# Kernel tuning notes

Hardware: AMD Instinct MI355X
Metric: run time of the kernel (lower is better)

## Reference

```python
import math
import jax, jax.numpy as jnp
import numpy as np

WIDTH = 24
LAYERS = 4
MODES = (12, 12, 12)
FOURIER_K = 8
EPS = 1e-5  # torch GroupNorm default


def _posenc(B, Z, Y, X, dtype):
    z = jnp.linspace(-1.0, 1.0, Z, dtype=dtype)
    y = jnp.linspace(-1.0, 1.0, Y, dtype=dtype)
    x = jnp.linspace(-1.0, 1.0, X, dtype=dtype)
    zz, yy, xx = jnp.meshgrid(z, y, x, indexing='ij')
    feats = [zz, yy, xx]
    for k in range(1, FOURIER_K + 1):
        w = k * math.pi
        feats += [jnp.sin(w * zz), jnp.cos(w * zz),
                  jnp.sin(w * yy), jnp.cos(w * yy),
                  jnp.sin(w * xx), jnp.cos(w * xx)]
    pe = jnp.stack(feats, axis=0)  # [3 + 6K, Z, Y, X]
    return jnp.broadcast_to(pe[None], (B,) + pe.shape)


def _conv1x1(h, w, b):
    # h: [B,C,Z,Y,X], w: [O,C], b: [O]
    return jnp.einsum('bczyx,oc->bozyx', h, w) + b[None, :, None, None, None]


def _spectral(h, w_ri):
    # h: [B,C,Z,Y,X], w_ri: [C,O,mz,my,mx,2]
    B, C, Z, Y, X = h.shape
    mz, my, mx = MODES
    hf = jnp.fft.rfftn(h, axes=(-3, -2, -1))  # [B,C,Z,Y,X//2+1] complex
    wc = w_ri[..., 0] + 1j * w_ri[..., 1]
    out = jnp.einsum('bczyx,cozyx->bozyx', hf[:, :, :mz, :my, :mx], wc)
    full = jnp.zeros((B, wc.shape[1], Z, Y, X // 2 + 1), dtype=out.dtype)
    full = full.at[:, :, :mz, :my, :mx].set(out)
    return jnp.fft.irfftn(full, s=(Z, Y, X), axes=(-3, -2, -1)).astype(h.dtype)


def _depthwise3(h, w, b):
    # depthwise 3x3x3 conv, padding 1; w: [C,1,3,3,3]
    out = jax.lax.conv_general_dilated(
        h, w, window_strides=(1, 1, 1), padding='SAME',
        dimension_numbers=('NCDHW', 'OIDHW', 'NCDHW'),
        feature_group_count=WIDTH)
    return out + b[None, :, None, None, None]


def _groupnorm1(h, g, b):
    # GroupNorm with num_groups=1: normalize over (C,Z,Y,X) per sample
    m = jnp.mean(h, axis=(1, 2, 3, 4), keepdims=True)
    v = jnp.var(h, axis=(1, 2, 3, 4), keepdims=True)
    hn = (h - m) * jax.lax.rsqrt(v + EPS)
    return hn * g[None, :, None, None, None] + b[None, :, None, None, None]


def setup_inputs() -> dict:
    key = jax.random.key(0)
    ks = jax.random.split(key, 16)
    B, C_IN, Z, Y, X = 4, 3, 64, 64, 64
    mz, my, mx = MODES
    extra_c = 3 + 6 * FOURIER_K
    scale = 1.0 / (WIDTH * WIDTH)
    inp = {
        'x': jax.random.normal(ks[0], (B, C_IN, Z, Y, X), jnp.float32),
        'lift_w': jax.random.normal(ks[1], (WIDTH, C_IN + extra_c), jnp.float32) * 0.1,
        'lift_b': jax.random.normal(ks[2], (WIDTH,), jnp.float32) * 0.01,
        'spec_w': jax.random.normal(ks[3], (LAYERS, WIDTH, WIDTH, mz, my, mx, 2), jnp.float32) * scale,
        'ws_w': jax.random.normal(ks[4], (LAYERS, WIDTH, WIDTH), jnp.float32) * 0.1,
        'ws_b': jax.random.normal(ks[5], (LAYERS, WIDTH), jnp.float32) * 0.01,
        'loc_w': jax.random.normal(ks[6], (LAYERS, WIDTH, 1, 3, 3, 3), jnp.float32) * 0.1,
        'loc_b': jax.random.normal(ks[7], (LAYERS, WIDTH), jnp.float32) * 0.01,
        'gn_w': jnp.ones((LAYERS, WIDTH), jnp.float32),
        'gn_b': jnp.zeros((LAYERS, WIDTH), jnp.float32),
        'gammas': jnp.full((LAYERS,), 0.5, jnp.float32),
        'proj1_w': jax.random.normal(ks[8], (WIDTH, WIDTH), jnp.float32) * 0.1,
        'proj1_b': jax.random.normal(ks[9], (WIDTH,), jnp.float32) * 0.01,
        'proj2_w': jax.random.normal(ks[10], (1, WIDTH), jnp.float32) * 0.1,
        'proj2_b': jnp.zeros((1,), jnp.float32),
    }
    return inp


def reference(x, lift_w, lift_b, spec_w, ws_w, ws_b, loc_w, loc_b,
              gn_w, gn_b, gammas, proj1_w, proj1_b, proj2_w, proj2_b):
    B, _, Z, Y, X = x.shape
    pe = _posenc(B, Z, Y, X, x.dtype)
    xin = jnp.concatenate([x, pe], axis=1)
    h = _conv1x1(xin, lift_w, lift_b)
    for i in range(LAYERS):
        y = _spectral(h, spec_w[i]) + _conv1x1(h, ws_w[i], ws_b[i]) + _depthwise3(h, loc_w[i], loc_b[i])
        y = jax.nn.gelu(y, approximate=False)
        h = h + gammas[i] * y
        h = _groupnorm1(h, gn_w[i], gn_b[i])
    p = jax.nn.gelu(_conv1x1(h, proj1_w, proj1_b), approximate=False)
    return _conv1x1(p, proj2_w, proj2_b)  # [B,1,Z,Y,X]
```

## Files before the change

### kernel.cpp

```cpp
#include <hip/hip_runtime.h>
#include <hip/hip_bf16.h>
#include <math.h>


static constexpr int BN = 4;
static constexpr int CW = 24;
static constexpr int ZD = 64;
static constexpr size_t NPTS = 64ull * 64 * 64;
static constexpr int KM = 12;
static constexpr int KK2 = 144;
static constexpr int M3 = 1728;
static constexpr int NLAYERS = 4;

static constexpr size_t OFF_H     = 0;
static constexpr size_t OFF_PRE   = OFF_H   + (size_t)BN * CW * NPTS;
static constexpr size_t OFF_A1    = OFF_PRE + (size_t)BN * CW * NPTS;
static constexpr size_t OFF_A2    = OFF_A1  + (size_t)BN * CW * ZD * KM * ZD * 2;
static constexpr size_t OFF_HF    = OFF_A2  + (size_t)BN * CW * KK2 * ZD * 2;
static constexpr size_t OFF_OUT   = OFF_HF  + (size_t)BN * CW * M3 * 2;
static constexpr size_t OFF_AX    = OFF_OUT + (size_t)BN * CW * M3 * 2;
static constexpr size_t OFF_STATS = OFF_AX  + 3 * CW * 64;
static constexpr size_t OFF_GWGB  = OFF_STATS + NLAYERS * BN * 2;

__device__ __forceinline__ float gelu_exact(float y) {
  return 0.5f * y * (1.f + erff(y * 0.70710678118654752f));
}

__global__ void k_axis(const float* __restrict__ lw, float* __restrict__ ws) {
  int t = blockIdx.x * blockDim.x + threadIdx.x;
  if (blockIdx.x == 0 && threadIdx.x < BN * CW) {
    ws[OFF_GWGB + threadIdx.x * 2]     = 1.f;
    ws[OFF_GWGB + threadIdx.x * 2 + 1] = 0.f;
  }
  if (t >= 3 * CW * 64) return;
  int v = t & 63;
  int o = (t >> 6) % CW;
  int axis = t / (64 * CW);
  float val = -1.f + 2.f * (float)v / 63.f;
  float acc = lw[o * 54 + 3 + axis] * val;
  for (int k = 1; k <= 8; k++) {
    float s, c;
    sincosf((float)k * 3.14159265358979323846f * val, &s, &c);
    int base = 6 + 6 * (k - 1) + 2 * axis;
    acc += lw[o * 54 + base] * s + lw[o * 54 + base + 1] * c;
  }
  ws[OFF_AX + (size_t)axis * CW * 64 + o * 64 + v] = acc;
}

__global__ __launch_bounds__(64) void k_lift(const float* __restrict__ xin,
                                             const float* __restrict__ lw,
                                             const float* __restrict__ lb,
                                             float* __restrict__ ws) {
  int bid = blockIdx.x;
  int b = bid >> 12, z = (bid >> 6) & 63, y = bid & 63;
  int tx = threadIdx.x;
  size_t zyx = (size_t)z * 4096 + y * 64 + tx;
  float x0 = xin[(size_t)(b * 3 + 0) * NPTS + zyx];
  float x1 = xin[(size_t)(b * 3 + 1) * NPTS + zyx];
  float x2 = xin[(size_t)(b * 3 + 2) * NPTS + zyx];
  const float* az = ws + OFF_AX;
  const float* ay = az + CW * 64;
  const float* axt = ay + CW * 64;
  float* h = ws + OFF_H;
  for (int o = 0; o < CW; o++) {
    float acc = lb[o] + lw[o * 54 + 0] * x0 + lw[o * 54 + 1] * x1 +
                lw[o * 54 + 2] * x2 + az[o * 64 + z] + ay[o * 64 + y] + axt[o * 64 + tx];
    h[(size_t)(b * CW + o) * NPTS + zyx] = acc;
  }
}

__global__ void k_dftx(const float* __restrict__ hsrc, float* __restrict__ A1,
                       const float* __restrict__ gwgb) {
  __shared__ float pl[64][65];
  int bid = blockIdx.x;
  int bc = bid >> 6;
  float gw = gwgb[bc * 2], gb = gwgb[bc * 2 + 1];
  const float* src = hsrc + (size_t)bid * 4096;
  int t = threadIdx.x;
  for (int i = t; i < 4096; i += 256) pl[i >> 6][i & 63] = fmaf(src[i], gw, gb);
  __syncthreads();
  int q = t >> 6, y = t & 63;
  float C0, S0, C1, S1, C2, S2;
  sincosf(-6.283185307179586f * (float)q / 64.f, &S0, &C0);
  sincosf(-6.283185307179586f * (float)(q + 4) / 64.f, &S1, &C1);
  sincosf(-6.283185307179586f * (float)(q + 8) / 64.f, &S2, &C2);
  float r0 = 1.f, i0 = 0.f, r1 = 1.f, i1 = 0.f, r2 = 1.f, i2 = 0.f;
  float ar0 = 0.f, ai0 = 0.f, ar1 = 0.f, ai1 = 0.f, ar2 = 0.f, ai2 = 0.f;
  const float* row = pl[y];
  for (int xx = 0; xx < 64; xx++) {
    float v = row[xx];
    ar0 = fmaf(v, r0, ar0); ai0 = fmaf(v, i0, ai0);
    ar1 = fmaf(v, r1, ar1); ai1 = fmaf(v, i1, ai1);
    ar2 = fmaf(v, r2, ar2); ai2 = fmaf(v, i2, ai2);
    float nr;
    nr = r0 * C0 - i0 * S0; i0 = fmaf(r0, S0, i0 * C0); r0 = nr;
    nr = r1 * C1 - i1 * S1; i1 = fmaf(r1, S1, i1 * C1); r1 = nr;
    nr = r2 * C2 - i2 * S2; i2 = fmaf(r2, S2, i2 * C2); r2 = nr;
  }
  float2* dst = (float2*)A1 + (size_t)bid * KM * 64;
  dst[t]       = make_float2(ar0, ai0);
  dst[t + 256] = make_float2(ar1, ai1);
  dst[t + 512] = make_float2(ar2, ai2);
}

__global__ void k_dfty(const float* __restrict__ A1, float* __restrict__ A2) {
  __shared__ float lre[12][65], lim[12][65];
  int bid = blockIdx.x;
  int z = bid & 63, bc = bid >> 6;
  const float2* src = (const float2*)A1 + (size_t)bid * KM * 64;
  int t = threadIdx.x;
  for (int i = t; i < 768; i += 256) { float2 v = src[i]; lre[i >> 6][i & 63] = v.x; lim[i >> 6][i & 63] = v.y; }
  __syncthreads();
  if (t < KK2) {
    int ky = t / 12, kx = t % 12;
    float C, S;
    sincosf(-6.283185307179586f * (float)ky / 64.f, &S, &C);
    float r = 1.f, ir = 0.f;
    float re = 0.f, im = 0.f;
    for (int y = 0; y < 64; y++) {
      float ar = lre[kx][y], ai = lim[kx][y];
      re += ar * r - ai * ir;
      im += ai * r + ar * ir;
      float nr = r * C - ir * S; ir = fmaf(r, S, ir * C); r = nr;
    }
    ((float2*)A2)[((size_t)bc * KK2 + t) * 64 + z] = make_float2(re, im);
  }
}

__global__ void k_dftz(const float* __restrict__ A2, float* __restrict__ Hf) {
  __shared__ float lre[12][65], lim[12][65];
  int bid = blockIdx.x;
  int ky = bid % 12, bc = bid / 12;
  const float2* src = (const float2*)A2 + ((size_t)bc * KK2 + ky * 12) * 64;
  int t = threadIdx.x;
  for (int i = t; i < 768; i += 256) { float2 v = src[i]; lre[i >> 6][i & 63] = v.x; lim[i >> 6][i & 63] = v.y; }
  __syncthreads();
  if (t < KK2) {
    int kz = t / 12, kx = t % 12;
    float C, S;
    sincosf(-6.283185307179586f * (float)kz / 64.f, &S, &C);
    float r = 1.f, ir = 0.f;
    float re = 0.f, im = 0.f;
    for (int zz = 0; zz < 64; zz++) {
      float ar = lre[kx][zz], ai = lim[kx][zz];
      re += ar * r - ai * ir;
      im += ai * r + ar * ir;
      float nr = r * C - ir * S; ir = fmaf(r, S, ir * C); r = nr;
    }
    ((float2*)Hf)[(size_t)bc * M3 + kz * KK2 + ky * 12 + kx] = make_float2(re, im);
  }
}

__global__ void k_mix(const float* __restrict__ Hf, const float* __restrict__ specw,
                      float* __restrict__ Outb, int layer) {
  __shared__ float hre[24][64], him[24][64];
  int bid = blockIdx.x;
  int b = bid / 54, rem = bid % 54;
  int chunk = rem >> 1, og = rem & 1;
  int m0 = chunk * 64;
  int t = threadIdx.x;
  const float2* hf = (const float2*)Hf + (size_t)b * CW * M3;
  for (int i = t; i < 24 * 64; i += 256) {
    int c = i >> 6, m = i & 63;
    float2 v = hf[(size_t)c * M3 + m0 + m];
    hre[c][m] = v.x; him[c][m] = v.y;
  }
  __syncthreads();
  const float2* W2 = (const float2*)specw + (size_t)layer * 576 * M3;
  float2* outp = (float2*)Outb + (size_t)b * CW * M3;
  for (int p = t; p < 12 * 64; p += 256) {
    int o = og * 12 + (p >> 6), m = p & 63;
    int mg = m0 + m;
    float re = 0.f, im = 0.f;
    for (int c = 0; c < 24; c++) {
      float2 w = W2[(size_t)(c * 24 + o) * M3 + mg];
      float wr = w.x, wi = w.y;
      float ar = hre[c][m], ai = him[c][m];
      re += ar * wr - ai * wi;
      im += ar * wi + ai * wr;
    }
    int kx = mg % 12;
    float sc = (kx == 0 ? 1.f : 2.f) * (1.f / 262144.f);
    outp[(size_t)o * M3 + mg] = make_float2(re * sc, im * sc);
  }
}

__global__ void k_invz(const float* __restrict__ Outb, float* __restrict__ B1) {
  __shared__ float lre[1728], lim[1728];
  int bid = blockIdx.x;
  int bo = bid >> 2, zc = bid & 3;
  const float2* src = (const float2*)Outb + (size_t)bo * M3;
  int t = threadIdx.x;
  for (int i = t; i < 1728; i += 256) { float2 v = src[i]; lre[i] = v.x; lim[i] = v.y; }
  __syncthreads();
  float2* dst = (float2*)B1 + (size_t)bo * 64 * KK2 + (size_t)zc * 16 * KK2;
  for (int p = t; p < 16 * KK2; p += 256) {
    int z = zc * 16 + p / KK2, kk = p % KK2;
    float C, S;
    sincosf(6.283185307179586f * (float)z / 64.f, &S, &C);
    float r = 1.f, ir = 0.f;
    float re = 0.f, im = 0.f;
    for (int kz = 0; kz < 12; kz++) {
      float ar = lre[kz * KK2 + kk], ai = lim[kz * KK2 + kk];
      re += ar * r - ai * ir;
      im += ar * ir + ai * r;
      float nr = r * C - ir * S; ir = fmaf(r, S, ir * C); r = nr;
    }
    dst[p] = make_float2(re, im);
  }
}

__global__ void k_invy(const float* __restrict__ B1, float* __restrict__ B2) {
  __shared__ float lre[144], lim[144];
  int bid = blockIdx.x;
  const float2* src = (const float2*)B1 + (size_t)bid * KK2;
  int t = threadIdx.x;
  if (t < 144) { float2 v = src[t]; lre[t] = v.x; lim[t] = v.y; }
  __syncthreads();
  float2* dst = (float2*)B2 + (size_t)bid * 64 * KM;
  for (int p = t; p < 64 * KM; p += 256) {
    int y = p / KM, kx = p % KM;
    float C, S;
    sincosf(6.283185307179586f * (float)y / 64.f, &S, &C);
    float r = 1.f, ir = 0.f;
    float re = 0.f, im = 0.f;
    for (int ky = 0; ky < 12; ky++) {
      float ar = lre[ky * 12 + kx], ai = lim[ky * 12 + kx];
      re += ar * r - ai * ir;
      im += ar * ir + ai * r;
      float nr = r * C - ir * S; ir = fmaf(r, S, ir * C); r = nr;
    }
    dst[p] = make_float2(re, im);
  }
}

__global__ __launch_bounds__(256) void k_layer(const float* __restrict__ hsrc,
                                               const float* __restrict__ B2f,
                                               const float* __restrict__ wsw,
                                               const float* __restrict__ wsb,
                                               const float* __restrict__ locw,
                                               const float* __restrict__ locb,
                                               const float* __restrict__ gammas,
                                               const float* __restrict__ gwgb,
                                               float* __restrict__ pre,
                                               float* __restrict__ stats, int layer) {
  __shared__ __align__(16) float s_ws[576];
  __shared__ float s_loc[648];
  __shared__ __align__(16) float s_sp[2304];
  __shared__ float s_wsb[24], s_locb[24];
  __shared__ float s_gw[24], s_gb[24];
  __shared__ float s_ch[2][18][66];
  __shared__ float s_red[8];

  int bid = blockIdx.x;
  int b = bid >> 10, z = (bid >> 4) & 63, yt = bid & 15;
  int y0 = yt * 4;
  int tid = threadIdx.x;
  int tx = tid & 63, ty = tid >> 6;
  int y = y0 + ty;

  for (int i = tid; i < 576; i += 256) s_ws[i] = wsw[layer * 576 + i];
  for (int i = tid; i < 648; i += 256) s_loc[i] = locw[layer * 648 + i];
  const float2* b2 = (const float2*)B2f;
  for (int i = tid; i < 1152; i += 256) {
    int o = i / 48, rem = i % 48;
    int tyy = rem / 12, kxx = rem % 12;
    float2 v = b2[(((size_t)(b * CW + o) * 64 + z) * 64 + (y0 + tyy)) * KM + kxx];
    s_sp[((o * 4 + tyy) * 12 + kxx) * 2]     = v.x;
    s_sp[((o * 4 + tyy) * 12 + kxx) * 2 + 1] = v.y;
  }
  if (tid < 24) {
    s_wsb[tid] = wsb[layer * 24 + tid]; s_locb[tid] = locb[layer * 24 + tid];
    s_gw[tid] = gwgb[(b * CW + tid) * 2]; s_gb[tid] = gwgb[(b * CW + tid) * 2 + 1];
  }
  if (tid < 72) {
    int bf = tid / 36, rem = tid % 36;
    s_ch[bf][rem >> 1][(rem & 1) * 65] = 0.f;
  }
  __syncthreads();

  float cs[12], sn[12];
#pragma unroll
  for (int k = 0; k < 12; k++) {
    sincosf(6.283185307179586f * (float)((k * tx) & 63) / 64.f, &sn[k], &cs[k]);
  }

  float gamma = gammas[layer];
  size_t base_b = (size_t)b * CW * NPTS;
  size_t zyx = (size_t)z * 4096 + (size_t)y * 64 + tx;

  float hreg[24];
#pragma unroll
  for (int c = 0; c < 24; c++) hreg[c] = fmaf(hsrc[base_b + (size_t)c * NPTS + zyx], s_gw[c], s_gb[c]);

  int si[5]; size_t sgo[5]; bool svalid[5];
#pragma unroll
  for (int j = 0; j < 5; j++) {
    int i = tid + j * 256;
    si[j] = i;
    int rr = i >> 6, xx = i & 63;
    int z2 = z + rr / 6 - 1, y2 = y0 + (rr % 6) - 1;
    svalid[j] = (i < 1152) && ((unsigned)z2 < 64u) && ((unsigned)y2 < 64u);
    sgo[j] = (size_t)((unsigned)z2 & 63u) * 4096 + (size_t)((unsigned)y2 & 63u) * 64 + xx;
  }

#pragma unroll
  for (int j = 0; j < 5; j++) {
    float v = svalid[j] ? fmaf(hsrc[base_b + sgo[j]], s_gw[0], s_gb[0]) : 0.f;
    if (si[j] < 1152) s_ch[0][si[j] >> 6][(si[j] & 63) + 1] = v;
  }
  __syncthreads();

  float lsum = 0.f, lsq = 0.f;
  int cur = 0;
  for (int o = 0; o < 24; o++) {
    float r0 = 0.f, r1 = 0.f, r2 = 0.f, r3 = 0.f, r4 = 0.f;
    if (o < 23) {
      size_t nb = base_b + (size_t)(o + 1) * NPTS;
      if (svalid[0]) r0 = hsrc[nb + sgo[0]];
      if (svalid[1]) r1 = hsrc[nb + sgo[1]];
      if (svalid[2]) r2 = hsrc[nb + sgo[2]];
      if (svalid[3]) r3 = hsrc[nb + sgo[3]];
      if (svalid[4]) r4 = hsrc[nb + sgo[4]];
    }

    float hc = s_ch[cur][7 + ty][1 + tx];
    float dv = 0.f;
#pragma unroll
    for (int zi = 0; zi < 3; zi++) {
#pragma unroll
      for (int yi = 0; yi < 3; yi++) {
        const float* row = &s_ch[cur][zi * 6 + ty + yi][1 + tx];
        int wb = (zi * 3 + yi) * 3;
        dv += row[-1] * s_loc[o * 27 + wb] + row[0] * s_loc[o * 27 + wb + 1] + row[1] * s_loc[o * 27 + wb + 2];
      }
    }
    const float4* wsv = (const float4*)&s_ws[o * 24];
    float4 wa0 = wsv[0], wa1 = wsv[1], wa2 = wsv[2], wa3 = wsv[3], wa4 = wsv[4], wa5 = wsv[5];
    float wv = wa0.x * hreg[0]  + wa0.y * hreg[1]  + wa0.z * hreg[2]  + wa0.w * hreg[3]
             + wa1.x * hreg[4]  + wa1.y * hreg[5]  + wa1.z * hreg[6]  + wa1.w * hreg[7]
             + wa2.x * hreg[8]  + wa2.y * hreg[9]  + wa2.z * hreg[10] + wa2.w * hreg[11]
             + wa3.x * hreg[12] + wa3.y * hreg[13] + wa3.z * hreg[14] + wa3.w * hreg[15]
             + wa4.x * hreg[16] + wa4.y * hreg[17] + wa4.z * hreg[18] + wa4.w * hreg[19]
             + wa5.x * hreg[20] + wa5.y * hreg[21] + wa5.z * hreg[22] + wa5.w * hreg[23];
    const float4* spv = (const float4*)&s_sp[(o * 4 + ty) * 24];
    float4 p0 = spv[0], p1 = spv[1], p2 = spv[2], p3 = spv[3], p4 = spv[4], p5 = spv[5];
    float sp = p0.x * cs[0]  - p0.y * sn[0]  + p0.z * cs[1]  - p0.w * sn[1]
             + p1.x * cs[2]  - p1.y * sn[2]  + p1.z * cs[3]  - p1.w * sn[3]
             + p2.x * cs[4]  - p2.y * sn[4]  + p2.z * cs[5]  - p2.w * sn[5]
             + p3.x * cs[6]  - p3.y * sn[6]  + p3.z * cs[7]  - p3.w * sn[7]
             + p4.x * cs[8]  - p4.y * sn[8]  + p4.z * cs[9]  - p4.w * sn[9]
             + p5.x * cs[10] - p5.y * sn[10] + p5.z * cs[11] - p5.w * sn[11];
    float yv = sp + wv + s_wsb[o] + dv + s_locb[o];
    float pv = hc + gamma * gelu_exact(yv);
    pre[base_b + (size_t)o * NPTS + zyx] = pv;
    lsum += pv; lsq += pv * pv;

    if (o < 23) {
      int nbuf = cur ^ 1;
      float gwn = s_gw[o + 1], gbn = s_gb[o + 1];
      float w0 = svalid[0] ? fmaf(r0, gwn, gbn) : 0.f;
      float w1 = svalid[1] ? fmaf(r1, gwn, gbn) : 0.f;
      float w2 = svalid[2] ? fmaf(r2, gwn, gbn) : 0.f;
      float w3 = svalid[3] ? fmaf(r3, gwn, gbn) : 0.f;
      float w4 = svalid[4] ? fmaf(r4, gwn, gbn) : 0.f;
      if (si[0] < 1152) s_ch[nbuf][si[0] >> 6][(si[0] & 63) + 1] = w0;
      if (si[1] < 1152) s_ch[nbuf][si[1] >> 6][(si[1] & 63) + 1] = w1;
      if (si[2] < 1152) s_ch[nbuf][si[2] >> 6][(si[2] & 63) + 1] = w2;
      if (si[3] < 1152) s_ch[nbuf][si[3] >> 6][(si[3] & 63) + 1] = w3;
      if (si[4] < 1152) s_ch[nbuf][si[4] >> 6][(si[4] & 63) + 1] = w4;
    }
    __syncthreads();
    cur ^= 1;
  }

  for (int off = 32; off; off >>= 1) { lsum += __shfl_down(lsum, off); lsq += __shfl_down(lsq, off); }
  if (tx == 0) { s_red[ty * 2] = lsum; s_red[ty * 2 + 1] = lsq; }
  __syncthreads();
  if (tid == 0) {
    float a = s_red[0] + s_red[2] + s_red[4] + s_red[6];
    float q = s_red[1] + s_red[3] + s_red[5] + s_red[7];
    atomicAdd(&stats[(layer * BN + b) * 2], a);
    atomicAdd(&stats[(layer * BN + b) * 2 + 1], q);
  }
}

__global__ void k_gnstat(const float* __restrict__ stats, float* __restrict__ gwgb,
                         const float* __restrict__ gnw, const float* __restrict__ gnb,
                         int layer) {
  __shared__ float s_m[BN], s_r[BN];
  int t = threadIdx.x;
  if (t < BN) {
    float s1 = stats[(layer * BN + t) * 2];
    float s2 = stats[(layer * BN + t) * 2 + 1];
    float n = (float)(CW * NPTS);
    float mean = s1 / n;
    float var = s2 / n - mean * mean;
    s_m[t] = mean; s_r[t] = rsqrtf(var + 1e-5f);
  }
  __syncthreads();
  if (t < BN * CW) {
    int b = t / CW, c = t % CW;
    float gw = gnw[layer * CW + c] * s_r[b];
    float gb = gnb[layer * CW + c] - s_m[b] * gw;
    gwgb[((size_t)(layer + 1) * BN * CW + t) * 2]     = gw;
    gwgb[((size_t)(layer + 1) * BN * CW + t) * 2 + 1] = gb;
  }
}

__global__ __launch_bounds__(64) void k_proj(const float* __restrict__ h,
                                             const float* __restrict__ p1w,
                                             const float* __restrict__ p1b,
                                             const float* __restrict__ p2w,
                                             const float* __restrict__ p2b,
                                             const float* __restrict__ gwgb,
                                             float* __restrict__ out) {
  __shared__ float s_w[576], s_b[24], s_w2[24], s_gw[24], s_gb[24];
  int bid = blockIdx.x;
  int b = bid >> 12, z = (bid >> 6) & 63, y = bid & 63;
  int tx = threadIdx.x;
  for (int i = tx; i < 576; i += 64) s_w[i] = p1w[i];
  if (tx < 24) {
    s_b[tx] = p1b[tx]; s_w2[tx] = p2w[tx];
    s_gw[tx] = gwgb[(b * CW + tx) * 2]; s_gb[tx] = gwgb[(b * CW + tx) * 2 + 1];
  }
  __syncthreads();
  size_t zyx = (size_t)z * 4096 + y * 64 + tx;
  size_t base_b = (size_t)b * CW * NPTS;
  float hreg[24];
  for (int c = 0; c < 24; c++) hreg[c] = fmaf(h[base_b + (size_t)c * NPTS + zyx], s_gw[c], s_gb[c]);
  float acc = p2b[0];
  for (int o = 0; o < 24; o++) {
    float t = s_b[o];
#pragma unroll
    for (int c = 0; c < 24; c++) t += s_w[o * 24 + c] * hreg[c];
    acc += s_w2[o] * gelu_exact(t);
  }
  out[(size_t)b * NPTS + zyx] = acc;
}

extern "C" void kernel_launch(void* const* d_in, const int* in_sizes, int n_in,
                              void* d_out, int out_size, void* d_ws, size_t ws_size,
                              hipStream_t stream) {
  const float* xin    = (const float*)d_in[0];
  const float* lift_w = (const float*)d_in[1];
  const float* lift_b = (const float*)d_in[2];
  const float* spec_w = (const float*)d_in[3];
  const float* ws_w   = (const float*)d_in[4];
  const float* ws_b   = (const float*)d_in[5];
  const float* loc_w  = (const float*)d_in[6];
  const float* loc_b  = (const float*)d_in[7];
  const float* gn_w   = (const float*)d_in[8];
  const float* gn_b   = (const float*)d_in[9];
  const float* gammas = (const float*)d_in[10];
  const float* p1w    = (const float*)d_in[11];
  const float* p1b    = (const float*)d_in[12];
  const float* p2w    = (const float*)d_in[13];
  const float* p2b    = (const float*)d_in[14];
  float* ws = (float*)d_ws;
  float* out = (float*)d_out;

  float* gwgb = ws + OFF_GWGB;
  float* state[2] = { ws + OFF_H, ws + OFF_PRE };

  hipMemsetAsync(ws + OFF_STATS, 0, (NLAYERS * BN * 2) * sizeof(float), stream);

  k_axis<<<18, 256, 0, stream>>>(lift_w, ws);
  k_lift<<<BN * 4096, 64, 0, stream>>>(xin, lift_w, lift_b, ws);

  for (int l = 0; l < NLAYERS; l++) {
    const float* src = state[l & 1];
    float* dst = state[(l & 1) ^ 1];
    const float* slot = gwgb + (size_t)l * BN * CW * 2;
    k_dftx<<<BN * CW * 64, 256, 0, stream>>>(src, ws + OFF_A1, slot);
    k_dfty<<<BN * CW * 64, 256, 0, stream>>>(ws + OFF_A1, ws + OFF_A2);
    k_dftz<<<BN * CW * 12, 256, 0, stream>>>(ws + OFF_A2, ws + OFF_HF);
    k_mix<<<BN * 54, 256, 0, stream>>>(ws + OFF_HF, spec_w, ws + OFF_OUT, l);
    k_invz<<<BN * CW * 4, 256, 0, stream>>>(ws + OFF_OUT, ws + OFF_A2);
    k_invy<<<BN * CW * 64, 256, 0, stream>>>(ws + OFF_A2, ws + OFF_A1);
    k_layer<<<BN * 1024, 256, 0, stream>>>(src, ws + OFF_A1, ws_w, ws_b, loc_w, loc_b,
                                           gammas, slot, dst, ws + OFF_STATS, l);
    k_gnstat<<<1, 128, 0, stream>>>(ws + OFF_STATS, gwgb, gn_w, gn_b, l);
  }
  k_proj<<<BN * 4096, 64, 0, stream>>>(state[0], p1w, p1b, p2w, p2b,
                                       gwgb + (size_t)NLAYERS * BN * CW * 2, out);
}
```

Baseline: 1.652 ms.

## Fuse y/z forward DFTs, inline GroupNorm affine, pair channels in layer kernel

Merges the separate y and z truncated-DFT kernels into one kernel that keeps the intermediate in shared memory, so the A2 global round trip and one launch go away. Drops the k_gnstat kernel and has each consumer compute the GroupNorm scale and shift directly from the accumulated stats. The layer kernel now handles two output channels per iteration with packed float2 weights and 4 staging buffers, which halves loop trips and barriers. The cost is more shared memory and registers per block in k_layer, plus redundant stat math in every block.

```diff
diff --git a/kernel.cpp b/kernel.cpp
--- a/kernel.cpp
+++ b/kernel.cpp
@@ -11,6 +11,10 @@
 static constexpr int KK2 = 144;
 static constexpr int M3 = 1728;
 static constexpr int NLAYERS = 4;
+static constexpr float GN_N = 6291456.0f;
+
+typedef float v2f __attribute__((ext_vector_type(2)));
+static __device__ __forceinline__ v2f mk2(float a, float b) { v2f r; r.x = a; r.y = b; return r; }
 
 static constexpr size_t OFF_H     = 0;
 static constexpr size_t OFF_PRE   = OFF_H   + (size_t)BN * CW * NPTS;
@@ -20,18 +24,28 @@
 static constexpr size_t OFF_OUT   = OFF_HF  + (size_t)BN * CW * M3 * 2;
 static constexpr size_t OFF_AX    = OFF_OUT + (size_t)BN * CW * M3 * 2;
 static constexpr size_t OFF_STATS = OFF_AX  + 3 * CW * 64;
-static constexpr size_t OFF_GWGB  = OFF_STATS + NLAYERS * BN * 2;
 
 __device__ __forceinline__ float gelu_exact(float y) {
   return 0.5f * y * (1.f + erff(y * 0.70710678118654752f));
 }
 
+__device__ __forceinline__ void gn_affine(const float* stats, const float* gnw,
+                                          const float* gnb, int lm1, int b, int c,
+                                          float& gw, float& gb) {
+  gw = 1.f; gb = 0.f;
+  if (lm1 >= 0) {
+    float s1 = stats[(lm1 * BN + b) * 2];
+    float s2 = stats[(lm1 * BN + b) * 2 + 1];
+    float mean = s1 / GN_N;
+    float var = s2 / GN_N - mean * mean;
+    float rstd = rsqrtf(var + 1e-5f);
+    gw = gnw[lm1 * CW + c] * rstd;
+    gb = gnb[lm1 * CW + c] - mean * gw;
+  }
+}
+
 __global__ void k_axis(const float* __restrict__ lw, float* __restrict__ ws) {
   int t = blockIdx.x * blockDim.x + threadIdx.x;
-  if (blockIdx.x == 0 && threadIdx.x < BN * CW) {
-    ws[OFF_GWGB + threadIdx.x * 2]     = 1.f;
-    ws[OFF_GWGB + threadIdx.x * 2 + 1] = 0.f;
-  }
   if (t >= 3 * CW * 64) return;
   int v = t & 63;
   int o = (t >> 6) % CW;
@@ -70,11 +84,13 @@
 }
 
 __global__ void k_dftx(const float* __restrict__ hsrc, float* __restrict__ A1,
-                       const float* __restrict__ gwgb) {
+                       const float* __restrict__ stats, const float* __restrict__ gnw,
+                       const float* __restrict__ gnb, int layer) {
   __shared__ float pl[64][65];
   int bid = blockIdx.x;
   int bc = bid >> 6;
-  float gw = gwgb[bc * 2], gb = gwgb[bc * 2 + 1];
+  float gw, gb;
+  gn_affine(stats, gnw, gnb, layer - 1, bc / CW, bc % CW, gw, gb);
   const float* src = hsrc + (size_t)bid * 4096;
   int t = threadIdx.x;
   for (int i = t; i < 4096; i += 256) pl[i >> 6][i & 63] = fmaf(src[i], gw, gb);
@@ -103,46 +119,42 @@
   dst[t + 512] = make_float2(ar2, ai2);
 }
 
-__global__ void k_dfty(const float* __restrict__ A1, float* __restrict__ A2) {
-  __shared__ float lre[12][65], lim[12][65];
-  int bid = blockIdx.x;
-  int z = bid & 63, bc = bid >> 6;
-  const float2* src = (const float2*)A1 + (size_t)bid * KM * 64;
+__global__ void k_dftyz(const float* __restrict__ A1, float* __restrict__ Hf) {
+  __shared__ float in_re[64][65], in_im[64][65];
+  __shared__ float o1_re[12][65], o1_im[12][65];
+  int bid = blockIdx.x;
+  int kx = bid % 12, bc = bid / 12;
   int t = threadIdx.x;
-  for (int i = t; i < 768; i += 256) { float2 v = src[i]; lre[i >> 6][i & 63] = v.x; lim[i >> 6][i & 63] = v.y; }
-  __syncthreads();
-  if (t < KK2) {
-    int ky = t / 12, kx = t % 12;
+  const float2* src = (const float2*)A1;
+  for (int i = t; i < 4096; i += 256) {
+    int z = i >> 6, y = i & 63;
+    float2 v = src[((size_t)(bc * 64 + z)) * 768 + kx * 64 + y];
+    in_re[z][y] = v.x; in_im[z][y] = v.y;
+  }
+  __syncthreads();
+  for (int i = t; i < 768; i += 256) {
+    int z = i / 12, ky = i % 12;
     float C, S;
     sincosf(-6.283185307179586f * (float)ky / 64.f, &S, &C);
     float r = 1.f, ir = 0.f;
     float re = 0.f, im = 0.f;
     for (int y = 0; y < 64; y++) {
-      float ar = lre[kx][y], ai = lim[kx][y];
+      float ar = in_re[z][y], ai = in_im[z][y];
       re += ar * r - ai * ir;
       im += ai * r + ar * ir;
       float nr = r * C - ir * S; ir = fmaf(r, S, ir * C); r = nr;
     }
-    ((float2*)A2)[((size_t)bc * KK2 + t) * 64 + z] = make_float2(re, im);
-  }
-}
-
-__global__ void k_dftz(const float* __restrict__ A2, float* __restrict__ Hf) {
-  __shared__ float lre[12][65], lim[12][65];
-  int bid = blockIdx.x;
-  int ky = bid % 12, bc = bid / 12;
-  const float2* src = (const float2*)A2 + ((size_t)bc * KK2 + ky * 12) * 64;
-  int t = threadIdx.x;
-  for (int i = t; i < 768; i += 256) { float2 v = src[i]; lre[i >> 6][i & 63] = v.x; lim[i >> 6][i & 63] = v.y; }
+    o1_re[ky][z] = re; o1_im[ky][z] = im;
+  }
   __syncthreads();
   if (t < KK2) {
-    int kz = t / 12, kx = t % 12;
+    int kz = t / 12, ky = t % 12;
     float C, S;
     sincosf(-6.283185307179586f * (float)kz / 64.f, &S, &C);
     float r = 1.f, ir = 0.f;
     float re = 0.f, im = 0.f;
     for (int zz = 0; zz < 64; zz++) {
-      float ar = lre[kx][zz], ai = lim[kx][zz];
+      float ar = o1_re[ky][zz], ai = o1_im[ky][zz];
       re += ar * r - ai * ir;
       im += ai * r + ar * ir;
       float nr = r * C - ir * S; ir = fmaf(r, S, ir * C); r = nr;
@@ -241,15 +253,15 @@
                                                const float* __restrict__ locw,
                                                const float* __restrict__ locb,
                                                const float* __restrict__ gammas,
-                                               const float* __restrict__ gwgb,
+                                               const float* __restrict__ gnw,
+                                               const float* __restrict__ gnb,
                                                float* __restrict__ pre,
                                                float* __restrict__ stats, int layer) {
-  __shared__ __align__(16) float s_ws[576];
-  __shared__ float s_loc[648];
-  __shared__ __align__(16) float s_sp[2304];
-  __shared__ float s_wsb[24], s_locb[24];
-  __shared__ float s_gw[24], s_gb[24];
-  __shared__ float s_ch[2][18][66];
+  __shared__ __align__(16) float s_ws2[576];
+  __shared__ __align__(8)  float s_loc2[1296];
+  __shared__ __align__(16) float s_sp2[2304];
+  __shared__ float s_wsb[24], s_locb[24], s_gw[24], s_gb[24];
+  __shared__ float s_ch[4][18][66];
   __shared__ float s_red[8];
 
   int bid = blockIdx.x;
@@ -259,21 +271,30 @@
   int tx = tid & 63, ty = tid >> 6;
   int y = y0 + ty;
 
-  for (int i = tid; i < 576; i += 256) s_ws[i] = wsw[layer * 576 + i];
-  for (int i = tid; i < 648; i += 256) s_loc[i] = locw[layer * 648 + i];
+  for (int i = tid; i < 576; i += 256) {
+    int o = i / 24, c = i % 24;
+    s_ws2[((o >> 1) * 24 + c) * 2 + (o & 1)] = wsw[layer * 576 + i];
+  }
+  for (int i = tid; i < 648; i += 256) {
+    int o = i / 27, tap = i % 27;
+    s_loc2[((o >> 1) * 27 + tap) * 2 + (o & 1)] = locw[layer * 648 + i];
+  }
   const float2* b2 = (const float2*)B2f;
   for (int i = tid; i < 1152; i += 256) {
     int o = i / 48, rem = i % 48;
     int tyy = rem / 12, kxx = rem % 12;
     float2 v = b2[(((size_t)(b * CW + o) * 64 + z) * 64 + (y0 + tyy)) * KM + kxx];
-    s_sp[((o * 4 + tyy) * 12 + kxx) * 2]     = v.x;
-    s_sp[((o * 4 + tyy) * 12 + kxx) * 2 + 1] = v.y;
+    int base = (((o >> 1) * 4 + tyy) * 12 + kxx) * 4;
+    s_sp2[base + (o & 1)]     = v.x;
+    s_sp2[base + 2 + (o & 1)] = v.y;
   }
   if (tid < 24) {
     s_wsb[tid] = wsb[layer * 24 + tid]; s_locb[tid] = locb[layer * 24 + tid];
-    s_gw[tid] = gwgb[(b * CW + tid) * 2]; s_gb[tid] = gwgb[(b * CW + tid) * 2 + 1];
-  }
-  if (tid < 72) {
+    float gw, gb;
+    gn_affine(stats, gnw, gnb, layer - 1, b, tid, gw, gb);
+    s_gw[tid] = gw; s_gb[tid] = gb;
+  }
+  if (tid < 144) {
     int bf = tid / 36, rem = tid % 36;
     s_ch[bf][rem >> 1][(rem & 1) * 65] = 0.f;
   }
@@ -306,72 +327,87 @@
 
 #pragma unroll
   for (int j = 0; j < 5; j++) {
-    float v = svalid[j] ? fmaf(hsrc[base_b + sgo[j]], s_gw[0], s_gb[0]) : 0.f;
-    if (si[j] < 1152) s_ch[0][si[j] >> 6][(si[j] & 63) + 1] = v;
+    float vA = svalid[j] ? fmaf(hsrc[base_b + sgo[j]], s_gw[0], s_gb[0]) : 0.f;
+    float vB = svalid[j] ? fmaf(hsrc[base_b + NPTS + sgo[j]], s_gw[1], s_gb[1]) : 0.f;
+    if (si[j] < 1152) {
+      s_ch[0][si[j] >> 6][(si[j] & 63) + 1] = vA;
+      s_ch[1][si[j] >> 6][(si[j] & 63) + 1] = vB;
+    }
   }
   __syncthreads();
 
   float lsum = 0.f, lsq = 0.f;
-  int cur = 0;
-  for (int o = 0; o < 24; o++) {
-    float r0 = 0.f, r1 = 0.f, r2 = 0.f, r3 = 0.f, r4 = 0.f;
-    if (o < 23) {
-      size_t nb = base_b + (size_t)(o + 1) * NPTS;
-      if (svalid[0]) r0 = hsrc[nb + sgo[0]];
-      if (svalid[1]) r1 = hsrc[nb + sgo[1]];
-      if (svalid[2]) r2 = hsrc[nb + sgo[2]];
-      if (svalid[3]) r3 = hsrc[nb + sgo[3]];
-      if (svalid[4]) r4 = hsrc[nb + sgo[4]];
-    }
-
-    float hc = s_ch[cur][7 + ty][1 + tx];
-    float dv = 0.f;
+#pragma unroll 1
+  for (int op = 0; op < 12; op++) {
+    int tb = (op & 1) * 2;
+    float r0=0.f,r1=0.f,r2=0.f,r3=0.f,r4=0.f,r5=0.f,r6=0.f,r7=0.f,r8=0.f,r9=0.f;
+    if (op < 11) {
+      size_t nbA = base_b + (size_t)(2 * op + 2) * NPTS;
+      size_t nbB = nbA + NPTS;
+      if (svalid[0]) { r0 = hsrc[nbA + sgo[0]]; r5 = hsrc[nbB + sgo[0]]; }
+      if (svalid[1]) { r1 = hsrc[nbA + sgo[1]]; r6 = hsrc[nbB + sgo[1]]; }
+      if (svalid[2]) { r2 = hsrc[nbA + sgo[2]]; r7 = hsrc[nbB + sgo[2]]; }
+      if (svalid[3]) { r3 = hsrc[nbA + sgo[3]]; r8 = hsrc[nbB + sgo[3]]; }
+      if (svalid[4]) { r4 = hsrc[nbA + sgo[4]]; r9 = hsrc[nbB + sgo[4]]; }
+    }
+
+    const float* t0 = &s_ch[tb][0][0];
+    const float* t1 = &s_ch[tb + 1][0][0];
+    v2f dv = mk2(0.f, 0.f), wv = mk2(0.f, 0.f), sp = mk2(0.f, 0.f);
 #pragma unroll
     for (int zi = 0; zi < 3; zi++) {
 #pragma unroll
       for (int yi = 0; yi < 3; yi++) {
-        const float* row = &s_ch[cur][zi * 6 + ty + yi][1 + tx];
-        int wb = (zi * 3 + yi) * 3;
-        dv += row[-1] * s_loc[o * 27 + wb] + row[0] * s_loc[o * 27 + wb + 1] + row[1] * s_loc[o * 27 + wb + 2];
+        int ro = (zi * 6 + ty + yi) * 66 + 1 + tx;
+        float a0m = t0[ro - 1], a00 = t0[ro], a0p = t0[ro + 1];
+        float a1m = t1[ro - 1], a10 = t1[ro], a1p = t1[ro + 1];
+        const v2f* lp = (const v2f*)&s_loc2[(op * 27 + (zi * 3 + yi) * 3) * 2];
+        dv += mk2(a0m, a1m) * lp[0];
+        dv += mk2(a00, a10) * lp[1];
+        dv += mk2(a0p, a1p) * lp[2];
       }
     }
-    const float4* wsv = (const float4*)&s_ws[o * 24];
-    float4 wa0 = wsv[0], wa1 = wsv[1], wa2 = wsv[2], wa3 = wsv[3], wa4 = wsv[4], wa5 = wsv[5];
-    float wv = wa0.x * hreg[0]  + wa0.y * hreg[1]  + wa0.z * hreg[2]  + wa0.w * hreg[3]
-             + wa1.x * hreg[4]  + wa1.y * hreg[5]  + wa1.z * hreg[6]  + wa1.w * hreg[7]
-             + wa2.x * hreg[8]  + wa2.y * hreg[9]  + wa2.z * hreg[10] + wa2.w * hreg[11]
-             + wa3.x * hreg[12] + wa3.y * hreg[13] + wa3.z * hreg[14] + wa3.w * hreg[15]
-             + wa4.x * hreg[16] + wa4.y * hreg[17] + wa4.z * hreg[18] + wa4.w * hreg[19]
-             + wa5.x * hreg[20] + wa5.y * hreg[21] + wa5.z * hreg[22] + wa5.w * hreg[23];
-    const float4* spv = (const float4*)&s_sp[(o * 4 + ty) * 24];
-    float4 p0 = spv[0], p1 = spv[1], p2 = spv[2], p3 = spv[3], p4 = spv[4], p5 = spv[5];
-    float sp = p0.x * cs[0]  - p0.y * sn[0]  + p0.z * cs[1]  - p0.w * sn[1]
-             + p1.x * cs[2]  - p1.y * sn[2]  + p1.z * cs[3]  - p1.w * sn[3]
-             + p2.x * cs[4]  - p2.y * sn[4]  + p2.z * cs[5]  - p2.w * sn[5]
-             + p3.x * cs[6]  - p3.y * sn[6]  + p3.z * cs[7]  - p3.w * sn[7]
-             + p4.x * cs[8]  - p4.y * sn[8]  + p4.z * cs[9]  - p4.w * sn[9]
-             + p5.x * cs[10] - p5.y * sn[10] + p5.z * cs[11] - p5.w * sn[11];
-    float yv = sp + wv + s_wsb[o] + dv + s_locb[o];
-    float pv = hc + gamma * gelu_exact(yv);
-    pre[base_b + (size_t)o * NPTS + zyx] = pv;
-    lsum += pv; lsq += pv * pv;
-
-    if (o < 23) {
-      int nbuf = cur ^ 1;
-      float gwn = s_gw[o + 1], gbn = s_gb[o + 1];
-      float w0 = svalid[0] ? fmaf(r0, gwn, gbn) : 0.f;
-      float w1 = svalid[1] ? fmaf(r1, gwn, gbn) : 0.f;
-      float w2 = svalid[2] ? fmaf(r2, gwn, gbn) : 0.f;
-      float w3 = svalid[3] ? fmaf(r3, gwn, gbn) : 0.f;
-      float w4 = svalid[4] ? fmaf(r4, gwn, gbn) : 0.f;
-      if (si[0] < 1152) s_ch[nbuf][si[0] >> 6][(si[0] & 63) + 1] = w0;
-      if (si[1] < 1152) s_ch[nbuf][si[1] >> 6][(si[1] & 63) + 1] = w1;
-      if (si[2] < 1152) s_ch[nbuf][si[2] >> 6][(si[2] & 63) + 1] = w2;
-      if (si[3] < 1152) s_ch[nbuf][si[3] >> 6][(si[3] & 63) + 1] = w3;
-      if (si[4] < 1152) s_ch[nbuf][si[4] >> 6][(si[4] & 63) + 1] = w4;
+    const v2f* wp = (const v2f*)&s_ws2[op * 48];
+#pragma unroll
+    for (int c = 0; c < 24; c++) wv += wp[c] * hreg[c];
+    const float4* spp = (const float4*)&s_sp2[(op * 4 + ty) * 48];
+#pragma unroll
+    for (int kx = 0; kx < 12; kx++) {
+      float4 q = spp[kx];
+      sp += mk2(q.x, q.y) * cs[kx];
+      sp -= mk2(q.z, q.w) * sn[kx];
+    }
+    int o0 = 2 * op, o1 = 2 * op + 1;
+    float hc0 = t0[(7 + ty) * 66 + 1 + tx];
+    float hc1 = t1[(7 + ty) * 66 + 1 + tx];
+    v2f yv = sp + wv + dv;
+    float pv0 = hc0 + gamma * gelu_exact(yv.x + s_wsb[o0] + s_locb[o0]);
+    float pv1 = hc1 + gamma * gelu_exact(yv.y + s_wsb[o1] + s_locb[o1]);
+    pre[base_b + (size_t)o0 * NPTS + zyx] = pv0;
+    pre[base_b + (size_t)o1 * NPTS + zyx] = pv1;
+    lsum += pv0 + pv1; lsq += pv0 * pv0 + pv1 * pv1;
+
+    if (op < 11) {
+      int nb = tb ^ 2;
+      float gwa = s_gw[o0 + 2], gba = s_gb[o0 + 2];
+      float gwb = s_gw[o1 + 2], gbb = s_gb[o1 + 2];
+      float wA0 = svalid[0] ? fmaf(r0, gwa, gba) : 0.f;
+      float wA1 = svalid[1] ? fmaf(r1, gwa, gba) : 0.f;
+      float wA2 = svalid[2] ? fmaf(r2, gwa, gba) : 0.f;
+      float wA3 = svalid[3] ? fmaf(r3, gwa, gba) : 0.f;
+      float wA4 = svalid[4] ? fmaf(r4, gwa, gba) : 0.f;
+      float wB0 = svalid[0] ? fmaf(r5, gwb, gbb) : 0.f;
+      float wB1 = svalid[1] ? fmaf(r6, gwb, gbb) : 0.f;
+      float wB2 = svalid[2] ? fmaf(r7, gwb, gbb) : 0.f;
+      float wB3 = svalid[3] ? fmaf(r8, gwb, gbb) : 0.f;
+      float wB4 = svalid[4] ? fmaf(r9, gwb, gbb) : 0.f;
+      if (si[0] < 1152) { s_ch[nb][si[0] >> 6][(si[0] & 63) + 1] = wA0; s_ch[nb + 1][si[0] >> 6][(si[0] & 63) + 1] = wB0; }
+      if (si[1] < 1152) { s_ch[nb][si[1] >> 6][(si[1] & 63) + 1] = wA1; s_ch[nb + 1][si[1] >> 6][(si[1] & 63) + 1] = wB1; }
+      if (si[2] < 1152) { s_ch[nb][si[2] >> 6][(si[2] & 63) + 1] = wA2; s_ch[nb + 1][si[2] >> 6][(si[2] & 63) + 1] = wB2; }
+      if (si[3] < 1152) { s_ch[nb][si[3] >> 6][(si[3] & 63) + 1] = wA3; s_ch[nb + 1][si[3] >> 6][(si[3] & 63) + 1] = wB3; }
+      if (si[4] < 1152) { s_ch[nb][si[4] >> 6][(si[4] & 63) + 1] = wA4; s_ch[nb + 1][si[4] >> 6][(si[4] & 63) + 1] = wB4; }
     }
     __syncthreads();
-    cur ^= 1;
   }
 
   for (int off = 32; off; off >>= 1) { lsum += __shfl_down(lsum, off); lsq += __shfl_down(lsq, off); }
@@ -385,35 +421,14 @@
   }
 }
 
-__global__ void k_gnstat(const float* __restrict__ stats, float* __restrict__ gwgb,
-                         const float* __restrict__ gnw, const float* __restrict__ gnb,
-                         int layer) {
-  __shared__ float s_m[BN], s_r[BN];
-  int t = threadIdx.x;
-  if (t < BN) {
-    float s1 = stats[(layer * BN + t) * 2];
-    float s2 = stats[(layer * BN + t) * 2 + 1];
-    float n = (float)(CW * NPTS);
-    float mean = s1 / n;
-    float var = s2 / n - mean * mean;
-    s_m[t] = mean; s_r[t] = rsqrtf(var + 1e-5f);
-  }
-  __syncthreads();
-  if (t < BN * CW) {
-    int b = t / CW, c = t % CW;
-    float gw = gnw[layer * CW + c] * s_r[b];
-    float gb = gnb[layer * CW + c] - s_m[b] * gw;
-    gwgb[((size_t)(layer + 1) * BN * CW + t) * 2]     = gw;
-    gwgb[((size_t)(layer + 1) * BN * CW + t) * 2 + 1] = gb;
-  }
-}
-
 __global__ __launch_bounds__(64) void k_proj(const float* __restrict__ h,
                                              const float* __restrict__ p1w,
                                              const float* __restrict__ p1b,
                                              const float* __restrict__ p2w,
                                              const float* __restrict__ p2b,
-                                             const float* __restrict__ gwgb,
+                                             const float* __restrict__ stats,
+                                             const float* __restrict__ gnw,
+                                             const float* __restrict__ gnb,
                                              float* __restrict__ out) {
   __shared__ float s_w[576], s_b[24], s_w2[24], s_gw[24], s_gb[24];
   int bid = blockIdx.x;
@@ -422,7 +437,9 @@
   for (int i = tx; i < 576; i += 64) s_w[i] = p1w[i];
   if (tx < 24) {
     s_b[tx] = p1b[tx]; s_w2[tx] = p2w[tx];
-    s_gw[tx] = gwgb[(b * CW + tx) * 2]; s_gb[tx] = gwgb[(b * CW + tx) * 2 + 1];
+    float gw, gb;
+    gn_affine(stats, gnw, gnb, NLAYERS - 1, b, tx, gw, gb);
+    s_gw[tx] = gw; s_gb[tx] = gb;
   }
   __syncthreads();
   size_t zyx = (size_t)z * 4096 + y * 64 + tx;
@@ -460,10 +477,10 @@
   float* ws = (float*)d_ws;
   float* out = (float*)d_out;
 
-  float* gwgb = ws + OFF_GWGB;
+  float* stats = ws + OFF_STATS;
   float* state[2] = { ws + OFF_H, ws + OFF_PRE };
 
-  hipMemsetAsync(ws + OFF_STATS, 0, (NLAYERS * BN * 2) * sizeof(float), stream);
+  hipMemsetAsync(stats, 0, (NLAYERS * BN * 2) * sizeof(float), stream);
 
   k_axis<<<18, 256, 0, stream>>>(lift_w, ws);
   k_lift<<<BN * 4096, 64, 0, stream>>>(xin, lift_w, lift_b, ws);
@@ -471,17 +488,14 @@
   for (int l = 0; l < NLAYERS; l++) {
     const float* src = state[l & 1];
     float* dst = state[(l & 1) ^ 1];
-    const float* slot = gwgb + (size_t)l * BN * CW * 2;
-    k_dftx<<<BN * CW * 64, 256, 0, stream>>>(src, ws + OFF_A1, slot);
-    k_dfty<<<BN * CW * 64, 256, 0, stream>>>(ws + OFF_A1, ws + OFF_A2);
-    k_dftz<<<BN * CW * 12, 256, 0, stream>>>(ws + OFF_A2, ws + OFF_HF);
+    k_dftx<<<BN * CW * 64, 256, 0, stream>>>(src, ws + OFF_A1, stats, gn_w, gn_b, l);
+    k_dftyz<<<BN * CW * 12, 256, 0, stream>>>(ws + OFF_A1, ws + OFF_HF);
     k_mix<<<BN * 54, 256, 0, stream>>>(ws + OFF_HF, spec_w, ws + OFF_OUT, l);
     k_invz<<<BN * CW * 4, 256, 0, stream>>>(ws + OFF_OUT, ws + OFF_A2);
     k_invy<<<BN * CW * 64, 256, 0, stream>>>(ws + OFF_A2, ws + OFF_A1);
     k_layer<<<BN * 1024, 256, 0, stream>>>(src, ws + OFF_A1, ws_w, ws_b, loc_w, loc_b,
-                                           gammas, slot, dst, ws + OFF_STATS, l);
-    k_gnstat<<<1, 128, 0, stream>>>(ws + OFF_STATS, gwgb, gn_w, gn_b, l);
+                                           gammas, gn_w, gn_b, dst, stats, l);
   }
   k_proj<<<BN * 4096, 64, 0, stream>>>(state[0], p1w, p1b, p2w, p2b,
-                                       gwgb + (size_t)NLAYERS * BN * CW * 2, out);
-}
+                                       stats, gn_w, gn_b, out);
+}
```

New measurement: 1.715 ms. 3.8% more time.

## Fuse y/z forward DFTs, inline GroupNorm affine, widen lift/proj blocks

Applied to the files above, without the earlier changes.

Merges the separate y- and z-direction truncated DFT kernels into one kernel that keeps the intermediate in shared memory, dropping the A2 round trip and one launch per layer. Removes the k_gnstat kernel by having each consumer compute the GroupNorm scale and shift directly from the accumulated stats. Widens the lift and projection kernels from 64-thread to 256-thread blocks. The fused DFT kernel launches only BN*CW*12 blocks that each hold a larger shared buffer, which may lower parallelism.

```diff
diff --git a/kernel.cpp b/kernel.cpp
--- a/kernel.cpp
+++ b/kernel.cpp
@@ -11,6 +11,7 @@
 static constexpr int KK2 = 144;
 static constexpr int M3 = 1728;
 static constexpr int NLAYERS = 4;
+static constexpr float GN_N = 6291456.0f;
 
 static constexpr size_t OFF_H     = 0;
 static constexpr size_t OFF_PRE   = OFF_H   + (size_t)BN * CW * NPTS;
@@ -20,18 +21,28 @@
 static constexpr size_t OFF_OUT   = OFF_HF  + (size_t)BN * CW * M3 * 2;
 static constexpr size_t OFF_AX    = OFF_OUT + (size_t)BN * CW * M3 * 2;
 static constexpr size_t OFF_STATS = OFF_AX  + 3 * CW * 64;
-static constexpr size_t OFF_GWGB  = OFF_STATS + NLAYERS * BN * 2;
 
 __device__ __forceinline__ float gelu_exact(float y) {
   return 0.5f * y * (1.f + erff(y * 0.70710678118654752f));
 }
 
+__device__ __forceinline__ void gn_affine(const float* stats, const float* gnw,
+                                          const float* gnb, int lm1, int b, int c,
+                                          float& gw, float& gb) {
+  gw = 1.f; gb = 0.f;
+  if (lm1 >= 0) {
+    float s1 = stats[(lm1 * BN + b) * 2];
+    float s2 = stats[(lm1 * BN + b) * 2 + 1];
+    float mean = s1 / GN_N;
+    float var = s2 / GN_N - mean * mean;
+    float rstd = rsqrtf(var + 1e-5f);
+    gw = gnw[lm1 * CW + c] * rstd;
+    gb = gnb[lm1 * CW + c] - mean * gw;
+  }
+}
+
 __global__ void k_axis(const float* __restrict__ lw, float* __restrict__ ws) {
   int t = blockIdx.x * blockDim.x + threadIdx.x;
-  if (blockIdx.x == 0 && threadIdx.x < BN * CW) {
-    ws[OFF_GWGB + threadIdx.x * 2]     = 1.f;
-    ws[OFF_GWGB + threadIdx.x * 2 + 1] = 0.f;
-  }
   if (t >= 3 * CW * 64) return;
   int v = t & 63;
   int o = (t >> 6) % CW;
@@ -47,13 +58,15 @@
   ws[OFF_AX + (size_t)axis * CW * 64 + o * 64 + v] = acc;
 }
 
-__global__ __launch_bounds__(64) void k_lift(const float* __restrict__ xin,
-                                             const float* __restrict__ lw,
-                                             const float* __restrict__ lb,
-                                             float* __restrict__ ws) {
-  int bid = blockIdx.x;
-  int b = bid >> 12, z = (bid >> 6) & 63, y = bid & 63;
-  int tx = threadIdx.x;
+__global__ __launch_bounds__(256) void k_lift(const float* __restrict__ xin,
+                                              const float* __restrict__ lw,
+                                              const float* __restrict__ lb,
+                                              float* __restrict__ ws) {
+  int bid = blockIdx.x;
+  int b = bid >> 10, z = (bid >> 4) & 63, yt = bid & 15;
+  int tid = threadIdx.x;
+  int tx = tid & 63, ty = tid >> 6;
+  int y = yt * 4 + ty;
   size_t zyx = (size_t)z * 4096 + y * 64 + tx;
   float x0 = xin[(size_t)(b * 3 + 0) * NPTS + zyx];
   float x1 = xin[(size_t)(b * 3 + 1) * NPTS + zyx];
@@ -70,11 +83,13 @@
 }
 
 __global__ void k_dftx(const float* __restrict__ hsrc, float* __restrict__ A1,
-                       const float* __restrict__ gwgb) {
+                       const float* __restrict__ stats, const float* __restrict__ gnw,
+                       const float* __restrict__ gnb, int layer) {
   __shared__ float pl[64][65];
   int bid = blockIdx.x;
   int bc = bid >> 6;
-  float gw = gwgb[bc * 2], gb = gwgb[bc * 2 + 1];
+  float gw, gb;
+  gn_affine(stats, gnw, gnb, layer - 1, bc / CW, bc % CW, gw, gb);
   const float* src = hsrc + (size_t)bid * 4096;
   int t = threadIdx.x;
   for (int i = t; i < 4096; i += 256) pl[i >> 6][i & 63] = fmaf(src[i], gw, gb);
@@ -103,46 +118,42 @@
   dst[t + 512] = make_float2(ar2, ai2);
 }
 
-__global__ void k_dfty(const float* __restrict__ A1, float* __restrict__ A2) {
-  __shared__ float lre[12][65], lim[12][65];
-  int bid = blockIdx.x;
-  int z = bid & 63, bc = bid >> 6;
-  const float2* src = (const float2*)A1 + (size_t)bid * KM * 64;
+__global__ void k_dftyz(const float* __restrict__ A1, float* __restrict__ Hf) {
+  __shared__ float in_re[64][65], in_im[64][65];
+  __shared__ float o1_re[12][65], o1_im[12][65];
+  int bid = blockIdx.x;
+  int kx = bid % 12, bc = bid / 12;
   int t = threadIdx.x;
-  for (int i = t; i < 768; i += 256) { float2 v = src[i]; lre[i >> 6][i & 63] = v.x; lim[i >> 6][i & 63] = v.y; }
-  __syncthreads();
-  if (t < KK2) {
-    int ky = t / 12, kx = t % 12;
+  const float2* src = (const float2*)A1;
+  for (int i = t; i < 4096; i += 256) {
+    int z = i >> 6, y = i & 63;
+    float2 v = src[((size_t)(bc * 64 + z)) * 768 + kx * 64 + y];
+    in_re[z][y] = v.x; in_im[z][y] = v.y;
+  }
+  __syncthreads();
+  for (int i = t; i < 768; i += 256) {
+    int z = i / 12, ky = i % 12;
     float C, S;
     sincosf(-6.283185307179586f * (float)ky / 64.f, &S, &C);
     float r = 1.f, ir = 0.f;
     float re = 0.f, im = 0.f;
     for (int y = 0; y < 64; y++) {
-      float ar = lre[kx][y], ai = lim[kx][y];
+      float ar = in_re[z][y], ai = in_im[z][y];
       re += ar * r - ai * ir;
       im += ai * r + ar * ir;
       float nr = r * C - ir * S; ir = fmaf(r, S, ir * C); r = nr;
     }
-    ((float2*)A2)[((size_t)bc * KK2 + t) * 64 + z] = make_float2(re, im);
-  }
-}
-
-__global__ void k_dftz(const float* __restrict__ A2, float* __restrict__ Hf) {
-  __shared__ float lre[12][65], lim[12][65];
-  int bid = blockIdx.x;
-  int ky = bid % 12, bc = bid / 12;
-  const float2* src = (const float2*)A2 + ((size_t)bc * KK2 + ky * 12) * 64;
-  int t = threadIdx.x;
-  for (int i = t; i < 768; i += 256) { float2 v = src[i]; lre[i >> 6][i & 63] = v.x; lim[i >> 6][i & 63] = v.y; }
+    o1_re[ky][z] = re; o1_im[ky][z] = im;
+  }
   __syncthreads();
   if (t < KK2) {
-    int kz = t / 12, kx = t % 12;
+    int kz = t / 12, ky = t % 12;
     float C, S;
     sincosf(-6.283185307179586f * (float)kz / 64.f, &S, &C);
     float r = 1.f, ir = 0.f;
     float re = 0.f, im = 0.f;
     for (int zz = 0; zz < 64; zz++) {
-      float ar = lre[kx][zz], ai = lim[kx][zz];
+      float ar = o1_re[ky][zz], ai = o1_im[ky][zz];
       re += ar * r - ai * ir;
       im += ai * r + ar * ir;
       float nr = r * C - ir * S; ir = fmaf(r, S, ir * C); r = nr;
@@ -241,7 +252,8 @@
                                                const float* __restrict__ locw,
                                                const float* __restrict__ locb,
                                                const float* __restrict__ gammas,
-                                               const float* __restrict__ gwgb,
+                                               const float* __restrict__ gnw,
+                                               const float* __restrict__ gnb,
                                                float* __restrict__ pre,
                                                float* __restrict__ stats, int layer) {
   __shared__ __align__(16) float s_ws[576];
@@ -271,7 +283,9 @@
   }
   if (tid < 24) {
     s_wsb[tid] = wsb[layer * 24 + tid]; s_locb[tid] = locb[layer * 24 + tid];
-    s_gw[tid] = gwgb[(b * CW + tid) * 2]; s_gb[tid] = gwgb[(b * CW + tid) * 2 + 1];
+    float gw, gb;
+    gn_affine(stats, gnw, gnb, layer - 1, b, tid, gw, gb);
+    s_gw[tid] = gw; s_gb[tid] = gb;
   }
   if (tid < 72) {
     int bf = tid / 36, rem = tid % 36;
@@ -385,49 +399,33 @@
   }
 }
 
-__global__ void k_gnstat(const float* __restrict__ stats, float* __restrict__ gwgb,
-                         const float* __restrict__ gnw, const float* __restrict__ gnb,
-                         int layer) {
-  __shared__ float s_m[BN], s_r[BN];
-  int t = threadIdx.x;
-  if (t < BN) {
-    float s1 = stats[(layer * BN + t) * 2];
-    float s2 = stats[(layer * BN + t) * 2 + 1];
-    float n = (float)(CW * NPTS);
-    float mean = s1 / n;
-    float var = s2 / n - mean * mean;
-    s_m[t] = mean; s_r[t] = rsqrtf(var + 1e-5f);
-  }
-  __syncthreads();
-  if (t < BN * CW) {
-    int b = t / CW, c = t % CW;
-    float gw = gnw[layer * CW + c] * s_r[b];
-    float gb = gnb[layer * CW + c] - s_m[b] * gw;
-    gwgb[((size_t)(layer + 1) * BN * CW + t) * 2]     = gw;
-    gwgb[((size_t)(layer + 1) * BN * CW + t) * 2 + 1] = gb;
-  }
-}
-
-__global__ __launch_bounds__(64) void k_proj(const float* __restrict__ h,
-                                             const float* __restrict__ p1w,
-                                             const float* __restrict__ p1b,
-                                             const float* __restrict__ p2w,
-                                             const float* __restrict__ p2b,
-                                             const float* __restrict__ gwgb,
-                                             float* __restrict__ out) {
+__global__ __launch_bounds__(256) void k_proj(const float* __restrict__ h,
+                                              const float* __restrict__ p1w,
+                                              const float* __restrict__ p1b,
+                                              const float* __restrict__ p2w,
+                                              const float* __restrict__ p2b,
+                                              const float* __restrict__ stats,
+                                              const float* __restrict__ gnw,
+                                              const float* __restrict__ gnb,
+                                              float* __restrict__ out) {
   __shared__ float s_w[576], s_b[24], s_w2[24], s_gw[24], s_gb[24];
   int bid = blockIdx.x;
-  int b = bid >> 12, z = (bid >> 6) & 63, y = bid & 63;
-  int tx = threadIdx.x;
-  for (int i = tx; i < 576; i += 64) s_w[i] = p1w[i];
-  if (tx < 24) {
-    s_b[tx] = p1b[tx]; s_w2[tx] = p2w[tx];
-    s_gw[tx] = gwgb[(b * CW + tx) * 2]; s_gb[tx] = gwgb[(b * CW + tx) * 2 + 1];
-  }
-  __syncthreads();
-  size_t zyx = (size_t)z * 4096 + y * 64 + tx;
+  int b = bid >> 10, z = (bid >> 4) & 63, yt = bid & 15;
+  int tid = threadIdx.x;
+  int tx = tid & 63, ty = tid >> 6;
+  int y = yt * 4 + ty;
+  for (int i = tid; i < 576; i += 256) s_w[i] = p1w[i];
+  if (tid < 24) {
+    s_b[tid] = p1b[tid]; s_w2[tid] = p2w[tid];
+    float gw, gb;
+    gn_affine(stats, gnw, gnb, NLAYERS - 1, b, tid, gw, gb);
+    s_gw[tid] = gw; s_gb[tid] = gb;
+  }
+  __syncthreads();
+  size_t zyx = (size_t)z * 4096 + (size_t)y * 64 + tx;
   size_t base_b = (size_t)b * CW * NPTS;
   float hreg[24];
+#pragma unroll
   for (int c = 0; c < 24; c++) hreg[c] = fmaf(h[base_b + (size_t)c * NPTS + zyx], s_gw[c], s_gb[c]);
   float acc = p2b[0];
   for (int o = 0; o < 24; o++) {
@@ -460,28 +458,25 @@
   float* ws = (float*)d_ws;
   float* out = (float*)d_out;
 
-  float* gwgb = ws + OFF_GWGB;
+  float* stats = ws + OFF_STATS;
   float* state[2] = { ws + OFF_H, ws + OFF_PRE };
 
-  hipMemsetAsync(ws + OFF_STATS, 0, (NLAYERS * BN * 2) * sizeof(float), stream);
+  hipMemsetAsync(stats, 0, (NLAYERS * BN * 2) * sizeof(float), stream);
 
   k_axis<<<18, 256, 0, stream>>>(lift_w, ws);
-  k_lift<<<BN * 4096, 64, 0, stream>>>(xin, lift_w, lift_b, ws);
+  k_lift<<<BN * 1024, 256, 0, stream>>>(xin, lift_w, lift_b, ws);
 
   for (int l = 0; l < NLAYERS; l++) {
     const float* src = state[l & 1];
     float* dst = state[(l & 1) ^ 1];
-    const float* slot = gwgb + (size_t)l * BN * CW * 2;
-    k_dftx<<<BN * CW * 64, 256, 0, stream>>>(src, ws + OFF_A1, slot);
-    k_dfty<<<BN * CW * 64, 256, 0, stream>>>(ws + OFF_A1, ws + OFF_A2);
-    k_dftz<<<BN * CW * 12, 256, 0, stream>>>(ws + OFF_A2, ws + OFF_HF);
+    k_dftx<<<BN * CW * 64, 256, 0, stream>>>(src, ws + OFF_A1, stats, gn_w, gn_b, l);
+    k_dftyz<<<BN * CW * 12, 256, 0, stream>>>(ws + OFF_A1, ws + OFF_HF);
     k_mix<<<BN * 54, 256, 0, stream>>>(ws + OFF_HF, spec_w, ws + OFF_OUT, l);
     k_invz<<<BN * CW * 4, 256, 0, stream>>>(ws + OFF_OUT, ws + OFF_A2);
     k_invy<<<BN * CW * 64, 256, 0, stream>>>(ws + OFF_A2, ws + OFF_A1);
     k_layer<<<BN * 1024, 256, 0, stream>>>(src, ws + OFF_A1, ws_w, ws_b, loc_w, loc_b,
-                                           gammas, slot, dst, ws + OFF_STATS, l);
-    k_gnstat<<<1, 128, 0, stream>>>(ws + OFF_STATS, gwgb, gn_w, gn_b, l);
-  }
-  k_proj<<<BN * 4096, 64, 0, stream>>>(state[0], p1w, p1b, p2w, p2b,
-                                       gwgb + (size_t)NLAYERS * BN * CW * 2, out);
-}
+                                           gammas, gn_w, gn_b, dst, stats, l);
+  }
+  k_proj<<<BN * 1024, 256, 0, stream>>>(state[0], p1w, p1b, p2w, p2b,
+                                        stats, gn_w, gn_b, out);
+}
```

Measured after the change: 1.583 ms. 1.04x faster.
